# Optimization experiments

Hardware: AMD Instinct MI355X
Metric: run time of the kernel (lower is better)

Reference implementation:

```python
import jax, jax.numpy as jnp
import numpy as np
from jax import lax

SIZE = 64
N_SUPPORT = 8192
N_QUERIES = 16384
UNROLLING_STEPS = 10


def setup_inputs() -> dict:
    key = jax.random.key(0)
    ks = jax.random.split(key, 6)
    s = 1.0 / np.sqrt(SIZE)
    return {
        "support": jax.random.normal(ks[0], (N_SUPPORT, SIZE), jnp.float32),
        "queries": jax.random.normal(ks[1], (N_QUERIES, SIZE), jnp.float32),
        "W_ih": jax.random.normal(ks[2], (4 * SIZE, SIZE), jnp.float32) * s,
        "W_hh": jax.random.normal(ks[3], (4 * SIZE, SIZE), jnp.float32) * s,
        "b_ih": jax.random.normal(ks[4], (4 * SIZE,), jnp.float32) * s,
        "b_hh": jax.random.normal(ks[5], (4 * SIZE,), jnp.float32) * s,
    }


def _lstm_cell(x, h, c, W_ih, W_hh, b_ih, b_hh):
    # PyTorch LSTMCell gate order: i, f, g, o
    gates = x @ W_ih.T + b_ih + h @ W_hh.T + b_hh  # [B, 4*size]
    i, f, g, o = jnp.split(gates, 4, axis=1)
    c_new = jax.nn.sigmoid(f) * c + jax.nn.sigmoid(i) * jnp.tanh(g)
    h_new = jax.nn.sigmoid(o) * jnp.tanh(c_new)
    return h_new, c_new


def reference(support, queries, W_ih, W_hh, b_ih, b_hh):
    def step(carry, _):
        h_hat, c = carry
        h = h_hat + queries                              # [B, size]
        att = jax.nn.softmax(h @ support.T, axis=1)      # [B, n_support]
        readout = att @ support                          # [B, size]
        h_hat2, c2 = _lstm_cell(queries, h + readout, c, W_ih, W_hh, b_ih, b_hh)
        return (h_hat2, c2), None

    init = (jnp.zeros_like(queries), jnp.zeros_like(queries))
    (h_hat, _), _ = lax.scan(step, init, None, length=UNROLLING_STEPS)
    return h_hat + queries
```

## Files before the change

### kernel.cpp

```cpp
#include <hip/hip_runtime.h>

using u16 = unsigned short;
using u32 = unsigned int;

#define NS 8192
#define NQ 16384
#define SZ 64
#define STEPS 10
#define TS 64
#define TSZ (TS * SZ)
#define NT (NS / TS)
#define NR (NT / 2)
#define L2E 1.44269504088896340736f

typedef __attribute__((ext_vector_type(8))) _Float16 f16x8;
typedef __attribute__((ext_vector_type(4))) float f32x4;

static __device__ __forceinline__ float ex2(float x) { float r; asm("v_exp_f32 %0, %1" : "=v"(r) : "v"(x)); return r; }
static __device__ __forceinline__ float rcp_(float x) { float r; asm("v_rcp_f32 %0, %1" : "=v"(r) : "v"(x)); return r; }

static __device__ __forceinline__ u16 hbits(_Float16 h) { union { _Float16 h; u16 u; } c; c.h = h; return c.u; }
static __device__ __forceinline__ u32 pk2(float lo, float hi) {
    return (u32)hbits((_Float16)lo) | ((u32)hbits((_Float16)hi) << 16);
}
static __device__ __forceinline__ f32x4 MMH(f16x8 a, f16x8 b, f32x4 c) {
    return __builtin_amdgcn_mfma_f32_16x16x32_f16(a, b, c, 0, 0, 0);
}
static __device__ __forceinline__ f16x8 LD(const void* p) { return *(const f16x8*)p; }
static __device__ __forceinline__ float sig(float x) { return rcp_(1.f + ex2(-L2E * x)); }
static __device__ __forceinline__ float tanh_(float x) {
    float e = ex2(-2.f * L2E * x);
    return (1.f - e) * rcp_(1.f + e);
}
static __device__ __forceinline__ void lds_fence() {
    asm volatile("s_waitcnt lgkmcnt(0)" ::: "memory");
    __builtin_amdgcn_sched_barrier(0);
}
static __device__ __forceinline__ void gload16(const void* g, void* l) {
    __builtin_amdgcn_global_load_lds(
        (const __attribute__((address_space(1))) void*)g,
        (__attribute__((address_space(3))) void*)l, 16, 0, 0);
}

__global__ void prep_kernel(const float* __restrict__ sup,
                            const float* __restrict__ Wih,
                            const float* __restrict__ Whh,
                            const float* __restrict__ bih,
                            const float* __restrict__ bhh,
                            u16* __restrict__ supH, u16* __restrict__ supL,
                            u16* __restrict__ supT,
                            u16* __restrict__ WiH, u16* __restrict__ WiL,
                            u16* __restrict__ WhH, u16* __restrict__ WhL,
                            float* __restrict__ bs) {
    int i = blockIdx.x * 256 + threadIdx.x;
    if (i < NS * SZ) {
        float v = sup[i];
        _Float16 hi = (_Float16)v;
        _Float16 lo = (_Float16)(v - (float)hi);
        supH[i] = hbits(hi);
        supL[i] = hbits(lo);
        int s = i >> 6, d = i & 63;
        supT[(s >> 6) * TSZ + d * TS + (s & 63)] = hbits(hi);
    }
    if (i < 4 * SZ * SZ) {
        float a = Wih[i]; _Float16 ah = (_Float16)a;
        WiH[i] = hbits(ah); WiL[i] = hbits((_Float16)(a - (float)ah));
        float b = Whh[i]; _Float16 bh = (_Float16)b;
        WhH[i] = hbits(bh); WhL[i] = hbits((_Float16)(b - (float)bh));
    }
    if (i < 4 * SZ) bs[i] = bih[i] + bhh[i];
}

__global__ __launch_bounds__(512, 2) void attlstm_kernel(
    const float* __restrict__ queries,
    const u16* __restrict__ supH, const u16* __restrict__ supL,
    const u16* __restrict__ supT,
    const u16* __restrict__ WiH, const u16* __restrict__ WiL,
    const u16* __restrict__ WhH, const u16* __restrict__ WhL,
    const float* __restrict__ bsum,
    float* __restrict__ out) {
    __shared__ __align__(16) u16 stage[4][3][TSZ];
    __shared__ __align__(16) u32 P_lds[8][512];
    __shared__ __align__(16) u16 hsl[4][2048];
    __shared__ __align__(16) float bs_lds[256];

    const int tid = threadIdx.x;
    const int w = tid >> 6;
    const int l = tid & 63;
    const int wq = w & 3;
    const int half = w >> 2;
    const int q = l & 15;
    const int g = l >> 4;
    const int qrow = blockIdx.x * 64 + wq * 16 + q;
    const u32 swz = (u32)(q & 7) << 4;
    const bool lead = (half == 0);

    if (tid < 256) bs_lds[tid] = bsum[tid];

    const int srcoff = (w * 8 + (l >> 3)) * SZ + ((l & 7) ^ (l >> 3)) * 8;
    const u16* abase[3] = {supH, supL, supT};
    char* hslb = (char*)&hsl[wq][0];
    char* pw = (char*)&P_lds[w][0];

    float qv[16], hh[16], cc[16];
    f16x8 qfh0, qfh1, qfl0, qfl1;
    if (lead) {
#pragma unroll
        for (int s4 = 0; s4 < 4; ++s4) {
            f32x4 v = *(const f32x4*)&queries[qrow * SZ + 16 * s4 + 4 * g];
#pragma unroll
            for (int jj = 0; jj < 4; ++jj) {
                qv[4 * s4 + jj] = v[jj];
                hh[4 * s4 + jj] = 0.f;
                cc[4 * s4 + jj] = 0.f;
            }
            _Float16 c0 = (_Float16)v[0], c1 = (_Float16)v[1], c2 = (_Float16)v[2], c3 = (_Float16)v[3];
            uint2 whi, wlo;
            whi.x = (u32)hbits(c0) | ((u32)hbits(c1) << 16);
            whi.y = (u32)hbits(c2) | ((u32)hbits(c3) << 16);
            wlo.x = pk2(v[0] - (float)c0, v[1] - (float)c1);
            wlo.y = pk2(v[2] - (float)c2, v[3] - (float)c3);
            u32 b = q * 128 + ((32u * s4 + 8u * g) ^ swz);
            *(uint2*)(hslb + b) = whi;
            *(uint2*)(hslb + 2048 + b) = wlo;
        }
        lds_fence();
        qfh0 = LD(hslb + q * 128 + ((16u * g) ^ swz));
        qfh1 = LD(hslb + q * 128 + ((16u * g + 64u) ^ swz));
        qfl0 = LD(hslb + 2048 + q * 128 + ((16u * g) ^ swz));
        qfl1 = LD(hslb + 2048 + q * 128 + ((16u * g + 64u) ^ swz));
    }

#pragma unroll 1
    for (int step = 0; step < STEPS; ++step) {
        if (lead) {
#pragma unroll
            for (int s4 = 0; s4 < 4; ++s4) {
                float h0 = hh[4 * s4 + 0] + qv[4 * s4 + 0];
                float h1 = hh[4 * s4 + 1] + qv[4 * s4 + 1];
                float h2 = hh[4 * s4 + 2] + qv[4 * s4 + 2];
                float h3 = hh[4 * s4 + 3] + qv[4 * s4 + 3];
                _Float16 a0 = (_Float16)h0, a1 = (_Float16)h1, a2 = (_Float16)h2, a3 = (_Float16)h3;
                uint2 whi, wlo;
                whi.x = (u32)hbits(a0) | ((u32)hbits(a1) << 16);
                whi.y = (u32)hbits(a2) | ((u32)hbits(a3) << 16);
                wlo.x = pk2(h0 - (float)a0, h1 - (float)a1);
                wlo.y = pk2(h2 - (float)a2, h3 - (float)a3);
                u32 b = q * 128 + ((32u * s4 + 8u * g) ^ swz);
                *(uint2*)(hslb + b) = whi;
                *(uint2*)(hslb + 2048 + b) = wlo;
            }
        }
        __syncthreads();
        const f16x8 bh0 = LD(hslb + q * 128 + ((16u * g) ^ swz));
        const f16x8 bh1 = LD(hslb + q * 128 + ((16u * g + 64u) ^ swz));
        const f16x8 bl0 = LD(hslb + 2048 + q * 128 + ((16u * g) ^ swz));
        const f16x8 bl1 = LD(hslb + 2048 + q * 128 + ((16u * g + 64u) ^ swz));

#pragma unroll
        for (int a = 0; a < 3; ++a) {
            gload16(abase[a] + 0 * TSZ + srcoff, &stage[0][a][w * 512]);
            gload16(abase[a] + 1 * TSZ + srcoff, &stage[1][a][w * 512]);
        }
        __syncthreads();

        float m = -1e30f, mL = -1.5e30f, lsum = 0.f;
        f32x4 Oa[4] = {{0, 0, 0, 0}, {0, 0, 0, 0}, {0, 0, 0, 0}, {0, 0, 0, 0}};

#pragma unroll 1
        for (int r = 0; r < NR; ++r) {
            const int bufc = (2 * r + half) & 3;
            if (r < NR - 1) {
                const int tA = 2 * r + 2, tB = 2 * r + 3;
#pragma unroll
                for (int a = 0; a < 3; ++a) {
                    gload16(abase[a] + tA * TSZ + srcoff, &stage[tA & 3][a][w * 512]);
                    gload16(abase[a] + tB * TSZ + srcoff, &stage[tB & 3][a][w * 512]);
                }
            }
            const char* sH = (const char*)&stage[bufc][0][0];
            const char* sL = (const char*)&stage[bufc][1][0];
            const char* sT = (const char*)&stage[bufc][2][0];
            f32x4 sv[4];
#pragma unroll
            for (int sub = 0; sub < 4; ++sub) {
                u32 rb = (u32)(16 * sub + q) * 128;
                f16x8 aH0 = LD(sH + rb + ((16u * g) ^ swz));
                f16x8 aH1 = LD(sH + rb + ((16u * g + 64u) ^ swz));
                f16x8 aL0 = LD(sL + rb + ((16u * g) ^ swz));
                f16x8 aL1 = LD(sL + rb + ((16u * g + 64u) ^ swz));
                f32x4 a = {0, 0, 0, 0};
                a = MMH(aH0, bh0, a); a = MMH(aH1, bh1, a);
                a = MMH(aH0, bl0, a); a = MMH(aH1, bl1, a);
                a = MMH(aL0, bh0, a); a = MMH(aL1, bh1, a);
                sv[sub] = a;
            }
            float tm = -1e30f;
#pragma unroll
            for (int sub = 0; sub < 4; ++sub)
                tm = fmaxf(tm, fmaxf(fmaxf(sv[sub][0], sv[sub][1]), fmaxf(sv[sub][2], sv[sub][3])));
            tm = fmaxf(tm, __shfl_xor(tm, 16));
            tm = fmaxf(tm, __shfl_xor(tm, 32));
            if (__any(tm > m + 5.5f)) {
                float mn = fmaxf(m, tm);
                float sc = ex2((m - mn) * L2E);
                lsum *= sc;
                Oa[0] *= sc; Oa[1] *= sc; Oa[2] *= sc; Oa[3] *= sc;
                m = mn; mL = m * L2E;
            }
#pragma unroll
            for (int sub = 0; sub < 4; ++sub) {
                float p0 = ex2(sv[sub][0] * L2E - mL);
                float p1 = ex2(sv[sub][1] * L2E - mL);
                float p2 = ex2(sv[sub][2] * L2E - mL);
                float p3 = ex2(sv[sub][3] * L2E - mL);
                lsum += (p0 + p1) + (p2 + p3);
                uint2 wv; wv.x = pk2(p0, p1); wv.y = pk2(p2, p3);
                *(uint2*)(pw + q * 128 + ((32u * sub + 8u * g) ^ swz)) = wv;
            }
            lds_fence();
#pragma unroll
            for (int c4 = 0; c4 < 2; ++c4) {
                u32 kb = (16u * g + 64u * c4) ^ swz;
                f16x8 pb = LD(pw + q * 128 + kb);
#pragma unroll
                for (int dsub = 0; dsub < 4; ++dsub) {
                    f16x8 aT = LD(sT + (u32)(16 * dsub + q) * 128 + kb);
                    Oa[dsub] = MMH(aT, pb, Oa[dsub]);
                }
            }
            __syncthreads();
        }
        lsum += __shfl_xor(lsum, 16);
        lsum += __shfl_xor(lsum, 32);

        float* mg = (float*)&stage[0][0][0];
        float* mine = mg + (u32)(w * 64 + l) * 20;
        *(f32x4*)(mine + 0) = Oa[0];
        *(f32x4*)(mine + 4) = Oa[1];
        *(f32x4*)(mine + 8) = Oa[2];
        *(f32x4*)(mine + 12) = Oa[3];
        mine[16] = m; mine[17] = lsum;
        __syncthreads();

        if (lead) {
            const float* oth = mg + (u32)((w + 4) * 64 + l) * 20;
            f32x4 Ob0 = *(const f32x4*)(oth + 0);
            f32x4 Ob1 = *(const f32x4*)(oth + 4);
            f32x4 Ob2 = *(const f32x4*)(oth + 8);
            f32x4 Ob3 = *(const f32x4*)(oth + 12);
            float mo = oth[16], lo_ = oth[17];
            float M = fmaxf(m, mo);
            float sA = ex2((m - M) * L2E), sB = ex2((mo - M) * L2E);
            lsum = lsum * sA + lo_ * sB;
            Oa[0] = Oa[0] * sA + Ob0 * sB;
            Oa[1] = Oa[1] * sA + Ob1 * sB;
            Oa[2] = Oa[2] * sA + Ob2 * sB;
            Oa[3] = Oa[3] * sA + Ob3 * sB;
            float inv = rcp_(lsum);

#pragma unroll
            for (int s4 = 0; s4 < 4; ++s4) {
                float r0 = hh[4 * s4 + 0] + qv[4 * s4 + 0] + Oa[s4][0] * inv;
                float r1 = hh[4 * s4 + 1] + qv[4 * s4 + 1] + Oa[s4][1] * inv;
                float r2 = hh[4 * s4 + 2] + qv[4 * s4 + 2] + Oa[s4][2] * inv;
                float r3 = hh[4 * s4 + 3] + qv[4 * s4 + 3] + Oa[s4][3] * inv;
                _Float16 a0 = (_Float16)r0, a1 = (_Float16)r1, a2 = (_Float16)r2, a3 = (_Float16)r3;
                uint2 whi, wlo;
                whi.x = (u32)hbits(a0) | ((u32)hbits(a1) << 16);
                whi.y = (u32)hbits(a2) | ((u32)hbits(a3) << 16);
                wlo.x = pk2(r0 - (float)a0, r1 - (float)a1);
                wlo.y = pk2(r2 - (float)a2, r3 - (float)a3);
                u32 b = q * 128 + ((32u * s4 + 8u * g) ^ swz);
                *(uint2*)(hslb + b) = whi;
                *(uint2*)(hslb + 2048 + b) = wlo;
            }
            lds_fence();
            const f16x8 rh0 = LD(hslb + q * 128 + ((16u * g) ^ swz));
            const f16x8 rh1 = LD(hslb + q * 128 + ((16u * g + 64u) ^ swz));
            const f16x8 rl0 = LD(hslb + 2048 + q * 128 + ((16u * g) ^ swz));
            const f16x8 rl1 = LD(hslb + 2048 + q * 128 + ((16u * g + 64u) ^ swz));

#pragma unroll
            for (int s4 = 0; s4 < 4; ++s4) {
                f32x4 ga[4];
#pragma unroll
                for (int ch = 0; ch < 4; ++ch) {
                    int u_ = 4 * ch + s4;
                    f32x4 a = *(const f32x4*)&bs_lds[16 * u_ + 4 * g];
                    const u16* wiH = WiH + (16 * u_ + q) * SZ + 8 * g;
                    const u16* wiL = WiL + (16 * u_ + q) * SZ + 8 * g;
                    const u16* whH = WhH + (16 * u_ + q) * SZ + 8 * g;
                    const u16* whL = WhL + (16 * u_ + q) * SZ + 8 * g;
                    f16x8 w0 = LD(wiH), w1 = LD(wiH + 32);
                    a = MMH(w0, qfh0, a); a = MMH(w1, qfh1, a);
                    a = MMH(w0, qfl0, a); a = MMH(w1, qfl1, a);
                    a = MMH(LD(wiL), qfh0, a); a = MMH(LD(wiL + 32), qfh1, a);
                    f16x8 v0 = LD(whH), v1 = LD(whH + 32);
                    a = MMH(v0, rh0, a); a = MMH(v1, rh1, a);
                    a = MMH(v0, rl0, a); a = MMH(v1, rl1, a);
                    a = MMH(LD(whL), rh0, a); a = MMH(LD(whL + 32), rh1, a);
                    ga[ch] = a;
                }
#pragma unroll
                for (int jj = 0; jj < 4; ++jj) {
                    int tt = 4 * s4 + jj;
                    float gi = sig(ga[0][jj]);
                    float gf = sig(ga[1][jj]);
                    float gg = tanh_(ga[2][jj]);
                    float go = sig(ga[3][jj]);
                    float cn = gf * cc[tt] + gi * gg;
                    cc[tt] = cn;
                    hh[tt] = go * tanh_(cn);
                }
            }
        }
    }

    if (lead) {
#pragma unroll
        for (int s4 = 0; s4 < 4; ++s4) {
            f32x4 v;
#pragma unroll
            for (int jj = 0; jj < 4; ++jj) v[jj] = hh[4 * s4 + jj] + qv[4 * s4 + jj];
            *(f32x4*)&out[qrow * SZ + 16 * s4 + 4 * g] = v;
        }
    }
}

extern "C" void kernel_launch(void* const* d_in, const int* in_sizes, int n_in,
                              void* d_out, int out_size, void* d_ws, size_t ws_size,
                              hipStream_t stream) {
    const float* support = (const float*)d_in[0];
    const float* queries = (const float*)d_in[1];
    const float* W_ih = (const float*)d_in[2];
    const float* W_hh = (const float*)d_in[3];
    const float* b_ih = (const float*)d_in[4];
    const float* b_hh = (const float*)d_in[5];
    float* out = (float*)d_out;

    u16* supH = (u16*)d_ws;
    u16* supL = supH + NS * SZ;
    u16* supT = supL + NS * SZ;
    u16* WiH = supT + NS * SZ;
    u16* WiL = WiH + 4 * SZ * SZ;
    u16* WhH = WiL + 4 * SZ * SZ;
    u16* WhL = WhH + 4 * SZ * SZ;
    float* bs = (float*)(WhL + 4 * SZ * SZ);

    prep_kernel<<<(NS * SZ) / 256, 256, 0, stream>>>(support, W_ih, W_hh, b_ih, b_hh,
                                                     supH, supL, supT, WiH, WiL, WhH, WhL, bs);
    attlstm_kernel<<<NQ / 64, 512, 0, stream>>>(queries, supH, supL, supT,
                                                WiH, WiL, WhH, WhL, bs, out);
}
```

Measured before the change: 1.435 ms.

## Split each support tile across two waves per query group using 1024-thread blocks

Blocks grow from 512 to 1024 threads, giving 16 waves: four per query group instead of two. Each pair of waves now shares a support tile, each handling half the scores and half the P·V reduction. The final online-softmax merge combines four partial accumulators instead of two. This raises parallelism and latency hiding per query block, at the cost of more LDS for P buffers, more synchronisation per round, and register pressure under the new launch bounds.

New measurement: 1.460 ms. About the same (+1.8%).

```diff
diff --git a/kernel.cpp b/kernel.cpp
--- a/kernel.cpp
+++ b/kernel.cpp
@@ -71,7 +71,7 @@
     if (i < 4 * SZ) bs[i] = bih[i] + bhh[i];
 }
 
-__global__ __launch_bounds__(512, 2) void attlstm_kernel(
+__global__ __launch_bounds__(1024, 4) void attlstm_kernel(
     const float* __restrict__ queries,
     const u16* __restrict__ supH, const u16* __restrict__ supL,
     const u16* __restrict__ supT,
@@ -80,26 +80,38 @@
     const float* __restrict__ bsum,
     float* __restrict__ out) {
     __shared__ __align__(16) u16 stage[4][3][TSZ];
-    __shared__ __align__(16) u32 P_lds[8][512];
+    __shared__ __align__(16) u32 P_lds[16][512];
     __shared__ __align__(16) u16 hsl[4][2048];
     __shared__ __align__(16) float bs_lds[256];
 
     const int tid = threadIdx.x;
     const int w = tid >> 6;
     const int l = tid & 63;
-    const int wq = w & 3;
-    const int half = w >> 2;
+    const int qg = w & 3;
+    const int quarter = w >> 2;
+    const int tsel = quarter >> 1;
+    const int shalf = quarter & 1;
+    const bool lead = (quarter == 0);
     const int q = l & 15;
     const int g = l >> 4;
-    const int qrow = blockIdx.x * 64 + wq * 16 + q;
+    const int qrow = blockIdx.x * 64 + qg * 16 + q;
     const u32 swz = (u32)(q & 7) << 4;
-    const bool lead = (half == 0);
 
     if (tid < 256) bs_lds[tid] = bsum[tid];
 
-    const int srcoff = (w * 8 + (l >> 3)) * SZ + ((l & 7) ^ (l >> 3)) * 8;
-    const u16* abase[3] = {supH, supL, supT};
-    char* hslb = (char*)&hsl[wq][0];
+    const u16* gsrc[3]; int inoff[3]; int ctsel[3];
+#pragma unroll
+    for (int j = 0; j < 3; ++j) {
+        int c = w + 16 * j;
+        ctsel[j] = c / 24;
+        int rem = c - 24 * ctsel[j];
+        int a = rem >> 3, s8 = rem & 7;
+        int srcoff = (s8 * 8 + (l >> 3)) * SZ + ((l & 7) ^ (l >> 3)) * 8;
+        gsrc[j] = ((a == 0) ? supH : (a == 1) ? supL : supT) + srcoff;
+        inoff[j] = a * TSZ + s8 * 512;
+    }
+    u16* stg = &stage[0][0][0];
+    char* hslb = (char*)&hsl[qg][0];
     char* pw = (char*)&P_lds[w][0];
 
     float qv[16], hh[16], cc[16];
@@ -158,10 +170,8 @@
         const f16x8 bl1 = LD(hslb + 2048 + q * 128 + ((16u * g + 64u) ^ swz));
 
 #pragma unroll
-        for (int a = 0; a < 3; ++a) {
-            gload16(abase[a] + 0 * TSZ + srcoff, &stage[0][a][w * 512]);
-            gload16(abase[a] + 1 * TSZ + srcoff, &stage[1][a][w * 512]);
-        }
+        for (int j = 0; j < 3; ++j)
+            gload16(gsrc[j] + ctsel[j] * TSZ, stg + ctsel[j] * 12288 + inoff[j]);
         __syncthreads();
 
         float m = -1e30f, mL = -1.5e30f, lsum = 0.f;
@@ -169,22 +179,21 @@
 
 #pragma unroll 1
         for (int r = 0; r < NR; ++r) {
-            const int bufc = (2 * r + half) & 3;
             if (r < NR - 1) {
-                const int tA = 2 * r + 2, tB = 2 * r + 3;
-#pragma unroll
-                for (int a = 0; a < 3; ++a) {
-                    gload16(abase[a] + tA * TSZ + srcoff, &stage[tA & 3][a][w * 512]);
-                    gload16(abase[a] + tB * TSZ + srcoff, &stage[tB & 3][a][w * 512]);
+#pragma unroll
+                for (int j = 0; j < 3; ++j) {
+                    int t = 2 * r + 2 + ctsel[j];
+                    gload16(gsrc[j] + t * TSZ, stg + (t & 3) * 12288 + inoff[j]);
                 }
             }
-            const char* sH = (const char*)&stage[bufc][0][0];
-            const char* sL = (const char*)&stage[bufc][1][0];
-            const char* sT = (const char*)&stage[bufc][2][0];
-            f32x4 sv[4];
-#pragma unroll
-            for (int sub = 0; sub < 4; ++sub) {
-                u32 rb = (u32)(16 * sub + q) * 128;
+            const int myslot = (2 * r + tsel) & 3;
+            const char* sH = (const char*)(stg + myslot * 12288);
+            const char* sL = sH + TSZ * 2;
+            const char* sT = sH + 2 * TSZ * 2;
+            f32x4 sv[2];
+#pragma unroll
+            for (int sub = 0; sub < 2; ++sub) {
+                u32 rb = (u32)(16 * (2 * shalf + sub) + q) * 128;
                 f16x8 aH0 = LD(sH + rb + ((16u * g) ^ swz));
                 f16x8 aH1 = LD(sH + rb + ((16u * g + 64u) ^ swz));
                 f16x8 aL0 = LD(sL + rb + ((16u * g) ^ swz));
@@ -195,10 +204,8 @@
                 a = MMH(aL0, bh0, a); a = MMH(aL1, bh1, a);
                 sv[sub] = a;
             }
-            float tm = -1e30f;
-#pragma unroll
-            for (int sub = 0; sub < 4; ++sub)
-                tm = fmaxf(tm, fmaxf(fmaxf(sv[sub][0], sv[sub][1]), fmaxf(sv[sub][2], sv[sub][3])));
+            float tm = fmaxf(fmaxf(fmaxf(sv[0][0], sv[0][1]), fmaxf(sv[0][2], sv[0][3])),
+                             fmaxf(fmaxf(sv[1][0], sv[1][1]), fmaxf(sv[1][2], sv[1][3])));
             tm = fmaxf(tm, __shfl_xor(tm, 16));
             tm = fmaxf(tm, __shfl_xor(tm, 32));
             if (__any(tm > m + 5.5f)) {
@@ -209,7 +216,7 @@
                 m = mn; mL = m * L2E;
             }
 #pragma unroll
-            for (int sub = 0; sub < 4; ++sub) {
+            for (int sub = 0; sub < 2; ++sub) {
                 float p0 = ex2(sv[sub][0] * L2E - mL);
                 float p1 = ex2(sv[sub][1] * L2E - mL);
                 float p2 = ex2(sv[sub][2] * L2E - mL);
@@ -219,22 +226,19 @@
                 *(uint2*)(pw + q * 128 + ((32u * sub + 8u * g) ^ swz)) = wv;
             }
             lds_fence();
-#pragma unroll
-            for (int c4 = 0; c4 < 2; ++c4) {
-                u32 kb = (16u * g + 64u * c4) ^ swz;
-                f16x8 pb = LD(pw + q * 128 + kb);
-#pragma unroll
-                for (int dsub = 0; dsub < 4; ++dsub) {
-                    f16x8 aT = LD(sT + (u32)(16 * dsub + q) * 128 + kb);
-                    Oa[dsub] = MMH(aT, pb, Oa[dsub]);
-                }
+            f16x8 pb = LD(pw + q * 128 + ((16u * g) ^ swz));
+            u32 kbT = (16u * g + 64u * shalf) ^ swz;
+#pragma unroll
+            for (int dsub = 0; dsub < 4; ++dsub) {
+                f16x8 aT = LD(sT + (u32)(16 * dsub + q) * 128 + kbT);
+                Oa[dsub] = MMH(aT, pb, Oa[dsub]);
             }
             __syncthreads();
         }
         lsum += __shfl_xor(lsum, 16);
         lsum += __shfl_xor(lsum, 32);
 
-        float* mg = (float*)&stage[0][0][0];
+        float* mg = (float*)stg;
         float* mine = mg + (u32)(w * 64 + l) * 20;
         *(f32x4*)(mine + 0) = Oa[0];
         *(f32x4*)(mine + 4) = Oa[1];
@@ -244,19 +248,23 @@
         __syncthreads();
 
         if (lead) {
-            const float* oth = mg + (u32)((w + 4) * 64 + l) * 20;
-            f32x4 Ob0 = *(const f32x4*)(oth + 0);
-            f32x4 Ob1 = *(const f32x4*)(oth + 4);
-            f32x4 Ob2 = *(const f32x4*)(oth + 8);
-            f32x4 Ob3 = *(const f32x4*)(oth + 12);
-            float mo = oth[16], lo_ = oth[17];
-            float M = fmaxf(m, mo);
-            float sA = ex2((m - M) * L2E), sB = ex2((mo - M) * L2E);
-            lsum = lsum * sA + lo_ * sB;
-            Oa[0] = Oa[0] * sA + Ob0 * sB;
-            Oa[1] = Oa[1] * sA + Ob1 * sB;
-            Oa[2] = Oa[2] * sA + Ob2 * sB;
-            Oa[3] = Oa[3] * sA + Ob3 * sB;
+#pragma unroll
+            for (int k = 1; k < 4; ++k) {
+                const float* oth = mg + (u32)((w + 4 * k) * 64 + l) * 20;
+                f32x4 Ob0 = *(const f32x4*)(oth + 0);
+                f32x4 Ob1 = *(const f32x4*)(oth + 4);
+                f32x4 Ob2 = *(const f32x4*)(oth + 8);
+                f32x4 Ob3 = *(const f32x4*)(oth + 12);
+                float mo = oth[16], lo_ = oth[17];
+                float M = fmaxf(m, mo);
+                float sA = ex2((m - M) * L2E), sB = ex2((mo - M) * L2E);
+                lsum = lsum * sA + lo_ * sB;
+                Oa[0] = Oa[0] * sA + Ob0 * sB;
+                Oa[1] = Oa[1] * sA + Ob1 * sB;
+                Oa[2] = Oa[2] * sA + Ob2 * sB;
+                Oa[3] = Oa[3] * sA + Ob3 * sB;
+                m = M;
+            }
             float inv = rcp_(lsum);
 
 #pragma unroll
@@ -350,6 +358,6 @@
 
     prep_kernel<<<(NS * SZ) / 256, 256, 0, stream>>>(support, W_ih, W_hh, b_ih, b_hh,
                                                      supH, supL, supT, WiH, WiL, WhH, WhL, bs);
-    attlstm_kernel<<<NQ / 64, 512, 0, stream>>>(queries, supH, supL, supT,
-                                                WiH, WiL, WhH, WhL, bs, out);
-}
+    attlstm_kernel<<<NQ / 64, 1024, 0, stream>>>(queries, supH, supL, supT,
+                                                 WiH, WiL, WhH, WhL, bs, out);
+}
```
